# Performance work log

Measured on AMD Instinct MI355X. Metric: run time of the kernel, lower is better.

Reference implementation:

```python
import jax, jax.numpy as jnp
import numpy as np

N_NODES = 100000   # vertices
N_HEDGES = 20000   # hyperedges
NNZ = 1600000      # incidence entries (avg vertex degree 16)
IN_FT = 128
OUT_FT = 128


def setup_inputs() -> dict:
    key = jax.random.key(0)
    ks = jax.random.split(key, 8)
    stdv = 1.0 / np.sqrt(OUT_FT)
    x = jax.random.normal(ks[0], (N_NODES, IN_FT), dtype=jnp.float32)
    weight = jax.random.uniform(ks[1], (IN_FT, OUT_FT), dtype=jnp.float32, minval=-stdv, maxval=stdv)
    bias = jax.random.uniform(ks[2], (OUT_FT,), dtype=jnp.float32, minval=-stdv, maxval=stdv)
    node_idx = jax.random.randint(ks[3], (NNZ,), 0, N_NODES, dtype=jnp.int32)
    edge_idx = jax.random.randint(ks[4], (NNZ,), 0, N_HEDGES, dtype=jnp.int32)
    h_val = jnp.ones((NNZ,), dtype=jnp.float32)
    dv_inv = jax.random.uniform(ks[5], (N_NODES,), dtype=jnp.float32, minval=0.01, maxval=1.0)
    de_inv = jax.random.uniform(ks[6], (N_HEDGES,), dtype=jnp.float32, minval=0.01, maxval=1.0)
    return {"x": x, "weight": weight, "bias": bias, "node_idx": node_idx,
            "edge_idx": edge_idx, "h_val": h_val, "dv_inv": dv_inv, "de_inv": de_inv}


def reference(x, weight, bias, node_idx, edge_idx, h_val, dv_inv, de_inv):
    # dense map: X W + b
    x_mapped = jnp.matmul(x, weight) + bias                      # [N, F]
    # vertex-side degree scaling
    x_norm = x_mapped * dv_inv[:, None]                          # [N, F]
    # E = H^T x_norm : scatter vertex rows into hyperedges (spmm with COO H)
    msgs = x_norm[node_idx] * h_val[:, None]                     # [nnz, F]
    E = jax.ops.segment_sum(msgs, edge_idx, num_segments=N_HEDGES)  # [M, F]
    # hyperedge-side degree scaling
    E2 = E * de_inv[:, None]                                     # [M, F]
    # F_out = H E2 : scatter hyperedge rows back to vertices
    msgs2 = E2[edge_idx] * h_val[:, None]                        # [nnz, F]
    F_out = jax.ops.segment_sum(msgs2, node_idx, num_segments=N_NODES)  # [N, F]
    y = F_out * dv_inv[:, None]
    return y + x_mapped
```

## Files before the change

### kernel.cpp

```cpp
#include <hip/hip_runtime.h>


#define F 128
#define NBE 256
#define NBN 64
#define M_E 20000
#define RB_N 25000
#define R_N 4

__global__ __launch_bounds__(512) void kA_e(const int* __restrict__ ei,
                                            int* __restrict__ part2, int nnz) {
    __shared__ int sh[M_E];
    int b = blockIdx.x, t = threadIdx.x;
    for (int k = t; k < M_E; k += 512) sh[k] = 0;
    __syncthreads();
    int ch = (nnz + NBE - 1) / NBE;
    int i0 = b * ch, i1 = i0 + ch < nnz ? i0 + ch : nnz;
    for (int i = i0 + t; i < i1; i += 512) atomicAdd(&sh[ei[i]], 1);
    __syncthreads();
    for (int k = t; k < M_E; k += 512) part2[(size_t)b * M_E + k] = sh[k];
}

__global__ __launch_bounds__(512) void kA_n(const int* __restrict__ ni,
                                            int* __restrict__ partN2, int nnz) {
    __shared__ int sh[RB_N];
    int b = blockIdx.x >> 2, r = blockIdx.x & 3, t = threadIdx.x;
    for (int k = t; k < RB_N; k += 512) sh[k] = 0;
    __syncthreads();
    int ch = (nnz + NBN - 1) / NBN;
    int i0 = b * ch, i1 = i0 + ch < nnz ? i0 + ch : nnz;
    int lo = r * RB_N;
    for (int i = i0 + t; i < i1; i += 512) {
        int lb = ni[i] - lo;
        if ((unsigned)lb < (unsigned)RB_N) atomicAdd(&sh[lb], 1);
    }
    __syncthreads();
    for (int k = t; k < RB_N; k += 512)
        partN2[((size_t)(r * NBN + b)) * RB_N + k] = sh[k];
}

__global__ void kB(int* __restrict__ part2, int* __restrict__ cnt, int bins, int nb) {
    int bin = blockIdx.x * blockDim.x + threadIdx.x;
    if (bin >= bins) return;
    int run = 0;
#pragma unroll 8
    for (int b = 0; b < nb; ++b) {
        size_t idx = (size_t)b * bins + bin;
        int v = part2[idx];
        part2[idx] = run;
        run += v;
    }
    cnt[bin] = run;
}

__global__ void k_scan1(const int* __restrict__ cnt, int* __restrict__ excl,
                        int* __restrict__ part, int n) {
    __shared__ int s[256];
    int t = threadIdx.x;
    int base = blockIdx.x * 1024 + t * 4;
    int v0 = (base + 0 < n) ? cnt[base + 0] : 0;
    int v1 = (base + 1 < n) ? cnt[base + 1] : 0;
    int v2 = (base + 2 < n) ? cnt[base + 2] : 0;
    int v3 = (base + 3 < n) ? cnt[base + 3] : 0;
    s[t] = v0 + v1 + v2 + v3;
    __syncthreads();
    for (int off = 1; off < 256; off <<= 1) {
        int add = (t >= off) ? s[t - off] : 0;
        __syncthreads();
        s[t] += add;
        __syncthreads();
    }
    int r = (t > 0) ? s[t - 1] : 0;
    if (base + 0 < n) excl[base + 0] = r; r += v0;
    if (base + 1 < n) excl[base + 1] = r; r += v1;
    if (base + 2 < n) excl[base + 2] = r; r += v2;
    if (base + 3 < n) excl[base + 3] = r;
    if (t == 255) part[blockIdx.x] = s[255];
}

__global__ void k_scan2(int* __restrict__ part, int n) {
    __shared__ int s[256];
    int t = threadIdx.x;
    s[t] = (t < n) ? part[t] : 0;
    __syncthreads();
    for (int off = 1; off < 256; off <<= 1) {
        int add = (t >= off) ? s[t - off] : 0;
        __syncthreads();
        s[t] += add;
        __syncthreads();
    }
    if (t < n) part[t] = (t > 0) ? s[t - 1] : 0;
}

__global__ void k_scan3(int* __restrict__ start, const int* __restrict__ part, int n) {
    int i = blockIdx.x * blockDim.x + threadIdx.x;
    if (i < n) start[i] += part[i >> 10];
}

__global__ __launch_bounds__(512) void kC_e(const int* __restrict__ ei, const int* __restrict__ ni,
                                            const float* __restrict__ hv, const float* __restrict__ dv,
                                            const int* __restrict__ start, const int* __restrict__ part2,
                                            int2* __restrict__ eslot, int nnz) {
    __shared__ int sh[M_E];
    int b = blockIdx.x, t = threadIdx.x;
    for (int k = t; k < M_E; k += 512)
        sh[k] = start[k] + part2[(size_t)b * M_E + k];
    __syncthreads();
    int ch = (nnz + NBE - 1) / NBE;
    int i0 = b * ch, i1 = i0 + ch < nnz ? i0 + ch : nnz;
    for (int i = i0 + t; i < i1; i += 512) {
        int e = ei[i], nd = ni[i];
        float v = hv[i] * dv[nd];
        int p = atomicAdd(&sh[e], 1);
        eslot[p] = make_int2(nd, __float_as_int(v));
    }
}

__global__ __launch_bounds__(512) void kC_n(const int* __restrict__ ei, const int* __restrict__ ni,
                                            const float* __restrict__ hv,
                                            const int* __restrict__ start, const int* __restrict__ partN2,
                                            int2* __restrict__ nslot, int nnz) {
    __shared__ int sh[RB_N];
    int b = blockIdx.x >> 2, r = blockIdx.x & 3, t = threadIdx.x;
    int lo = r * RB_N;
    for (int k = t; k < RB_N; k += 512)
        sh[k] = start[lo + k] + partN2[((size_t)(r * NBN + b)) * RB_N + k];
    __syncthreads();
    int ch = (nnz + NBN - 1) / NBN;
    int i0 = b * ch, i1 = i0 + ch < nnz ? i0 + ch : nnz;
    for (int i = i0 + t; i < i1; i += 512) {
        int lb = ni[i] - lo;
        if ((unsigned)lb < (unsigned)RB_N) {
            int e = ei[i];
            float h = hv[i];
            int p = atomicAdd(&sh[lb], 1);
            nslot[p] = make_int2(e, __float_as_int(h));
        }
    }
}

__device__ __forceinline__ float f4_get(const float4& v, int k) {
    return k == 0 ? v.x : k == 1 ? v.y : k == 2 ? v.z : v.w;
}

__global__ __launch_bounds__(256) void k_gemm(const float* __restrict__ x,
                                              const float* __restrict__ w,
                                              const float* __restrict__ bias,
                                              float* __restrict__ y, int N) {
    __shared__ float sw[32 * 128];
    __shared__ float sx[128 * 36];
    int t = threadIdx.x;
    int row0 = blockIdx.x * 128;
    int cg = (t & 15) * 8;
    int rg = (t >> 4) * 8;
    float acc[8][8];
#pragma unroll
    for (int a = 0; a < 8; a++)
#pragma unroll
        for (int b = 0; b < 8; b++) acc[a][b] = 0.f;

    const float4* x4 = (const float4*)x;
    const float4* w4 = (const float4*)w;

    for (int kc = 0; kc < 4; ++kc) {
        __syncthreads();
        for (int i = t; i < 1024; i += 256) {
            int k = i >> 5, c4 = i & 31;
            ((float4*)sw)[i] = w4[(kc * 32 + k) * 32 + c4];
        }
        for (int i = t; i < 1024; i += 256) {
            int r = i >> 3, c4 = i & 7;
            float4 vv = make_float4(0.f, 0.f, 0.f, 0.f);
            if (row0 + r < N) vv = x4[(size_t)(row0 + r) * 32 + kc * 8 + c4];
            *(float4*)&sx[r * 36 + c4 * 4] = vv;
        }
        __syncthreads();
#pragma unroll
        for (int k4 = 0; k4 < 8; ++k4) {
            float4 xa[8];
#pragma unroll
            for (int rr = 0; rr < 8; rr++)
                xa[rr] = *(const float4*)&sx[(rg + rr) * 36 + k4 * 4];
#pragma unroll
            for (int kk = 0; kk < 4; kk++) {
                float4 wa0 = *(const float4*)&sw[(k4 * 4 + kk) * 128 + cg];
                float4 wa1 = *(const float4*)&sw[(k4 * 4 + kk) * 128 + cg + 4];
#pragma unroll
                for (int rr = 0; rr < 8; rr++) {
                    float xv = f4_get(xa[rr], kk);
                    acc[rr][0] += xv * wa0.x; acc[rr][1] += xv * wa0.y;
                    acc[rr][2] += xv * wa0.z; acc[rr][3] += xv * wa0.w;
                    acc[rr][4] += xv * wa1.x; acc[rr][5] += xv * wa1.y;
                    acc[rr][6] += xv * wa1.z; acc[rr][7] += xv * wa1.w;
                }
            }
        }
    }

    float4 b0 = *(const float4*)&bias[cg];
    float4 b1 = *(const float4*)&bias[cg + 4];
#pragma unroll
    for (int rr = 0; rr < 8; rr++) {
        int r = row0 + rg + rr;
        if (r < N) {
            float4 o0 = make_float4(acc[rr][0] + b0.x, acc[rr][1] + b0.y,
                                    acc[rr][2] + b0.z, acc[rr][3] + b0.w);
            float4 o1 = make_float4(acc[rr][4] + b1.x, acc[rr][5] + b1.y,
                                    acc[rr][6] + b1.z, acc[rr][7] + b1.w);
            *(float4*)&y[(size_t)r * F + cg]     = o0;
            *(float4*)&y[(size_t)r * F + cg + 4] = o1;
        }
    }
}

__global__ __launch_bounds__(256) void k_edge(const float* __restrict__ xm,
                                              const int2* __restrict__ slot,
                                              const float* __restrict__ de,
                                              const int* __restrict__ start,
                                              const int* __restrict__ cnt,
                                              float* __restrict__ E2, int M) {
    int wid = blockIdx.x * 4 + (threadIdx.x >> 6);
    if (wid >= M) return;
    int lane = threadIdx.x & 63;
    int hl = lane >> 5;
    int l  = lane & 31;
    int p = start[wid], c = cnt[wid];
    float a0 = 0.f, a1 = 0.f, a2 = 0.f, a3 = 0.f;
    int j = hl;
    for (; j + 2 < c; j += 4) {
        int2 s0 = slot[p + j];
        int2 s1 = slot[p + j + 2];
        float c0 = __int_as_float(s0.y), c1 = __int_as_float(s1.y);
        float4 v0 = *(const float4*)(xm + (size_t)s0.x * F + l * 4);
        float4 v1 = *(const float4*)(xm + (size_t)s1.x * F + l * 4);
        a0 += c0 * v0.x + c1 * v1.x;
        a1 += c0 * v0.y + c1 * v1.y;
        a2 += c0 * v0.z + c1 * v1.z;
        a3 += c0 * v0.w + c1 * v1.w;
    }
    if (j < c) {
        int2 s0 = slot[p + j];
        float c0 = __int_as_float(s0.y);
        float4 v0 = *(const float4*)(xm + (size_t)s0.x * F + l * 4);
        a0 += c0 * v0.x; a1 += c0 * v0.y; a2 += c0 * v0.z; a3 += c0 * v0.w;
    }
    a0 += __shfl_xor(a0, 32);
    a1 += __shfl_xor(a1, 32);
    a2 += __shfl_xor(a2, 32);
    a3 += __shfl_xor(a3, 32);
    if (hl == 0) {
        float s = de[wid];
        *(float4*)(E2 + (size_t)wid * F + l * 4) =
            make_float4(a0 * s, a1 * s, a2 * s, a3 * s);
    }
}

__global__ __launch_bounds__(256) void k_node(const float* xm,
                                              const int2* __restrict__ slot,
                                              const float* __restrict__ dv,
                                              const int* __restrict__ start,
                                              const int* __restrict__ cnt,
                                              const float* __restrict__ E2,
                                              float* out, int N) {
    int wid = blockIdx.x * 4 + (threadIdx.x >> 6);
    if (wid >= N) return;
    int lane = threadIdx.x & 63;
    int hl = lane >> 5;
    int l  = lane & 31;
    int p = start[wid], c = cnt[wid];
    float a0 = 0.f, a1 = 0.f, a2 = 0.f, a3 = 0.f;
    int j = hl;
    for (; j + 2 < c; j += 4) {
        int2 s0 = slot[p + j];
        int2 s1 = slot[p + j + 2];
        float c0 = __int_as_float(s0.y), c1 = __int_as_float(s1.y);
        float4 v0 = *(const float4*)(E2 + (size_t)s0.x * F + l * 4);
        float4 v1 = *(const float4*)(E2 + (size_t)s1.x * F + l * 4);
        a0 += c0 * v0.x + c1 * v1.x;
        a1 += c0 * v0.y + c1 * v1.y;
        a2 += c0 * v0.z + c1 * v1.z;
        a3 += c0 * v0.w + c1 * v1.w;
    }
    if (j < c) {
        int2 s0 = slot[p + j];
        float c0 = __int_as_float(s0.y);
        float4 v0 = *(const float4*)(E2 + (size_t)s0.x * F + l * 4);
        a0 += c0 * v0.x; a1 += c0 * v0.y; a2 += c0 * v0.z; a3 += c0 * v0.w;
    }
    a0 += __shfl_xor(a0, 32);
    a1 += __shfl_xor(a1, 32);
    a2 += __shfl_xor(a2, 32);
    a3 += __shfl_xor(a3, 32);
    if (hl == 0) {
        float dvn = dv[wid];
        float4 xv = *(const float4*)(xm + (size_t)wid * F + l * 4);
        *(float4*)(out + (size_t)wid * F + l * 4) =
            make_float4(a0 * dvn + xv.x, a1 * dvn + xv.y,
                        a2 * dvn + xv.z, a3 * dvn + xv.w);
    }
}

extern "C" void kernel_launch(void* const* d_in, const int* in_sizes, int n_in,
                              void* d_out, int out_size, void* d_ws, size_t ws_size,
                              hipStream_t stream) {
    const float* x      = (const float*)d_in[0];
    const float* w      = (const float*)d_in[1];
    const float* bias   = (const float*)d_in[2];
    const int*   ni     = (const int*)d_in[3];
    const int*   ei     = (const int*)d_in[4];
    const float* hv     = (const float*)d_in[5];
    const float* dv     = (const float*)d_in[6];
    const float* de     = (const float*)d_in[7];
    float* out = (float*)d_out;

    const int N   = in_sizes[0] / F;
    const int NNZ = in_sizes[3];
    const int M   = in_sizes[7];

    int* wsp        = (int*)d_ws;
    int* edge_cnt   = wsp;
    int* node_cnt   = edge_cnt + M;
    int* edge_start = node_cnt + N;
    int* node_start = edge_start + M;
    int* partE      = node_start + N;
    int* partN      = partE + 256;
    int* partE2     = partN + 256;
    int* partN2     = partE2 + (size_t)NBE * M_E;
    int2* eslot     = (int2*)(partN2 + (size_t)R_N * NBN * RB_N);
    int2* nslot     = eslot + NNZ;
    float* E2       = (float*)partN2;

    const int gScanE = (M + 1023) / 1024;
    const int gScanN = (N + 1023) / 1024;

    k_gemm<<<(N + 127) / 128, 256, 0, stream>>>(x, w, bias, out, N);

    kA_e<<<NBE, 512, 0, stream>>>(ei, partE2, NNZ);
    kA_n<<<NBN * R_N, 512, 0, stream>>>(ni, partN2, NNZ);

    kB<<<(M + 255) / 256, 256, 0, stream>>>(partE2, edge_cnt, M, NBE);
    for (int r = 0; r < R_N; ++r)
        kB<<<(RB_N + 255) / 256, 256, 0, stream>>>(partN2 + (size_t)r * NBN * RB_N,
                                                   node_cnt + (size_t)r * RB_N, RB_N, NBN);

    k_scan1<<<gScanE, 256, 0, stream>>>(edge_cnt, edge_start, partE, M);
    k_scan1<<<gScanN, 256, 0, stream>>>(node_cnt, node_start, partN, N);
    k_scan2<<<1, 256, 0, stream>>>(partE, gScanE);
    k_scan2<<<1, 256, 0, stream>>>(partN, gScanN);
    k_scan3<<<(M + 255) / 256, 256, 0, stream>>>(edge_start, partE, M);
    k_scan3<<<(N + 255) / 256, 256, 0, stream>>>(node_start, partN, N);

    kC_e<<<NBE, 512, 0, stream>>>(ei, ni, hv, dv, edge_start, partE2, eslot, NNZ);
    kC_n<<<NBN * R_N, 512, 0, stream>>>(ei, ni, hv, node_start, partN2, nslot, NNZ);

    k_edge<<<(M + 3) / 4, 256, 0, stream>>>(out, eslot, de, edge_start, edge_cnt, E2, M);
    k_node<<<(N + 3) / 4, 256, 0, stream>>>(out, nslot, dv, node_start, node_cnt, E2, out, N);
}
```

Measured before the change: 588.9 us.

## Gather bf16 copies of mapped features and edge sums in the SpMM passes

The GEMM now also writes a bf16 copy of X W + b, and the edge and node gather kernels read bf16 rows instead of fp32, which halves the bytes moved by the irregular gathers. The edge-pass output E2 is stored as bf16 too. To make room in the workspace, the GEMM launch moves after the CSR build and the edge histogram block count drops from 256 to 128. The risk is lost accuracy from bf16 rounding of the intermediates against the fp32 reference.

```diff
diff --git a/kernel.cpp b/kernel.cpp
--- a/kernel.cpp
+++ b/kernel.cpp
@@ -2,11 +2,20 @@
 
 
 #define F 128
-#define NBE 256
+#define NBE 128
 #define NBN 64
 #define M_E 20000
 #define RB_N 25000
 #define R_N 4
+
+__device__ __forceinline__ unsigned short f2bf(float f) {
+    unsigned u = __float_as_uint(f);
+    unsigned r = (u + 0x7FFF + ((u >> 16) & 1)) >> 16;
+    return (unsigned short)r;
+}
+__device__ __forceinline__ float bf2f(unsigned short h) {
+    return __uint_as_float((unsigned)h << 16);
+}
 
 __global__ __launch_bounds__(512) void kA_e(const int* __restrict__ ei,
                                             int* __restrict__ part2, int nnz) {
@@ -146,7 +155,8 @@
 __global__ __launch_bounds__(256) void k_gemm(const float* __restrict__ x,
                                               const float* __restrict__ w,
                                               const float* __restrict__ bias,
-                                              float* __restrict__ y, int N) {
+                                              float* __restrict__ y,
+                                              unsigned short* __restrict__ xmb, int N) {
     __shared__ float sw[32 * 128];
     __shared__ float sx[128 * 36];
     int t = threadIdx.x;
@@ -203,22 +213,26 @@
     for (int rr = 0; rr < 8; rr++) {
         int r = row0 + rg + rr;
         if (r < N) {
-            float4 o0 = make_float4(acc[rr][0] + b0.x, acc[rr][1] + b0.y,
-                                    acc[rr][2] + b0.z, acc[rr][3] + b0.w);
-            float4 o1 = make_float4(acc[rr][4] + b1.x, acc[rr][5] + b1.y,
-                                    acc[rr][6] + b1.z, acc[rr][7] + b1.w);
-            *(float4*)&y[(size_t)r * F + cg]     = o0;
-            *(float4*)&y[(size_t)r * F + cg + 4] = o1;
-        }
-    }
-}
-
-__global__ __launch_bounds__(256) void k_edge(const float* __restrict__ xm,
+            float o[8] = {acc[rr][0] + b0.x, acc[rr][1] + b0.y,
+                          acc[rr][2] + b0.z, acc[rr][3] + b0.w,
+                          acc[rr][4] + b1.x, acc[rr][5] + b1.y,
+                          acc[rr][6] + b1.z, acc[rr][7] + b1.w};
+            *(float4*)&y[(size_t)r * F + cg]     = make_float4(o[0], o[1], o[2], o[3]);
+            *(float4*)&y[(size_t)r * F + cg + 4] = make_float4(o[4], o[5], o[6], o[7]);
+            ushort4 h0 = {f2bf(o[0]), f2bf(o[1]), f2bf(o[2]), f2bf(o[3])};
+            ushort4 h1 = {f2bf(o[4]), f2bf(o[5]), f2bf(o[6]), f2bf(o[7])};
+            *(ushort4*)&xmb[(size_t)r * F + cg]     = h0;
+            *(ushort4*)&xmb[(size_t)r * F + cg + 4] = h1;
+        }
+    }
+}
+
+__global__ __launch_bounds__(256) void k_edge(const unsigned short* __restrict__ xmb,
                                               const int2* __restrict__ slot,
                                               const float* __restrict__ de,
                                               const int* __restrict__ start,
                                               const int* __restrict__ cnt,
-                                              float* __restrict__ E2, int M) {
+                                              unsigned short* __restrict__ E2b, int M) {
     int wid = blockIdx.x * 4 + (threadIdx.x >> 6);
     if (wid >= M) return;
     int lane = threadIdx.x & 63;
@@ -231,18 +245,19 @@
         int2 s0 = slot[p + j];
         int2 s1 = slot[p + j + 2];
         float c0 = __int_as_float(s0.y), c1 = __int_as_float(s1.y);
-        float4 v0 = *(const float4*)(xm + (size_t)s0.x * F + l * 4);
-        float4 v1 = *(const float4*)(xm + (size_t)s1.x * F + l * 4);
-        a0 += c0 * v0.x + c1 * v1.x;
-        a1 += c0 * v0.y + c1 * v1.y;
-        a2 += c0 * v0.z + c1 * v1.z;
-        a3 += c0 * v0.w + c1 * v1.w;
+        ushort4 v0 = *(const ushort4*)(xmb + (size_t)s0.x * F + l * 4);
+        ushort4 v1 = *(const ushort4*)(xmb + (size_t)s1.x * F + l * 4);
+        a0 += c0 * bf2f(v0.x) + c1 * bf2f(v1.x);
+        a1 += c0 * bf2f(v0.y) + c1 * bf2f(v1.y);
+        a2 += c0 * bf2f(v0.z) + c1 * bf2f(v1.z);
+        a3 += c0 * bf2f(v0.w) + c1 * bf2f(v1.w);
     }
     if (j < c) {
         int2 s0 = slot[p + j];
         float c0 = __int_as_float(s0.y);
-        float4 v0 = *(const float4*)(xm + (size_t)s0.x * F + l * 4);
-        a0 += c0 * v0.x; a1 += c0 * v0.y; a2 += c0 * v0.z; a3 += c0 * v0.w;
+        ushort4 v0 = *(const ushort4*)(xmb + (size_t)s0.x * F + l * 4);
+        a0 += c0 * bf2f(v0.x); a1 += c0 * bf2f(v0.y);
+        a2 += c0 * bf2f(v0.z); a3 += c0 * bf2f(v0.w);
     }
     a0 += __shfl_xor(a0, 32);
     a1 += __shfl_xor(a1, 32);
@@ -250,17 +265,16 @@
     a3 += __shfl_xor(a3, 32);
     if (hl == 0) {
         float s = de[wid];
-        *(float4*)(E2 + (size_t)wid * F + l * 4) =
-            make_float4(a0 * s, a1 * s, a2 * s, a3 * s);
-    }
-}
-
-__global__ __launch_bounds__(256) void k_node(const float* xm,
+        ushort4 o = {f2bf(a0 * s), f2bf(a1 * s), f2bf(a2 * s), f2bf(a3 * s)};
+        *(ushort4*)(E2b + (size_t)wid * F + l * 4) = o;
+    }
+}
+
+__global__ __launch_bounds__(256) void k_node(const unsigned short* __restrict__ E2b,
                                               const int2* __restrict__ slot,
                                               const float* __restrict__ dv,
                                               const int* __restrict__ start,
                                               const int* __restrict__ cnt,
-                                              const float* __restrict__ E2,
                                               float* out, int N) {
     int wid = blockIdx.x * 4 + (threadIdx.x >> 6);
     if (wid >= N) return;
@@ -274,18 +288,19 @@
         int2 s0 = slot[p + j];
         int2 s1 = slot[p + j + 2];
         float c0 = __int_as_float(s0.y), c1 = __int_as_float(s1.y);
-        float4 v0 = *(const float4*)(E2 + (size_t)s0.x * F + l * 4);
-        float4 v1 = *(const float4*)(E2 + (size_t)s1.x * F + l * 4);
-        a0 += c0 * v0.x + c1 * v1.x;
-        a1 += c0 * v0.y + c1 * v1.y;
-        a2 += c0 * v0.z + c1 * v1.z;
-        a3 += c0 * v0.w + c1 * v1.w;
+        ushort4 v0 = *(const ushort4*)(E2b + (size_t)s0.x * F + l * 4);
+        ushort4 v1 = *(const ushort4*)(E2b + (size_t)s1.x * F + l * 4);
+        a0 += c0 * bf2f(v0.x) + c1 * bf2f(v1.x);
+        a1 += c0 * bf2f(v0.y) + c1 * bf2f(v1.y);
+        a2 += c0 * bf2f(v0.z) + c1 * bf2f(v1.z);
+        a3 += c0 * bf2f(v0.w) + c1 * bf2f(v1.w);
     }
     if (j < c) {
         int2 s0 = slot[p + j];
         float c0 = __int_as_float(s0.y);
-        float4 v0 = *(const float4*)(E2 + (size_t)s0.x * F + l * 4);
-        a0 += c0 * v0.x; a1 += c0 * v0.y; a2 += c0 * v0.z; a3 += c0 * v0.w;
+        ushort4 v0 = *(const ushort4*)(E2b + (size_t)s0.x * F + l * 4);
+        a0 += c0 * bf2f(v0.x); a1 += c0 * bf2f(v0.y);
+        a2 += c0 * bf2f(v0.z); a3 += c0 * bf2f(v0.w);
     }
     a0 += __shfl_xor(a0, 32);
     a1 += __shfl_xor(a1, 32);
@@ -293,7 +308,7 @@
     a3 += __shfl_xor(a3, 32);
     if (hl == 0) {
         float dvn = dv[wid];
-        float4 xv = *(const float4*)(xm + (size_t)wid * F + l * 4);
+        float4 xv = *(const float4*)(out + (size_t)wid * F + l * 4);
         *(float4*)(out + (size_t)wid * F + l * 4) =
             make_float4(a0 * dvn + xv.x, a1 * dvn + xv.y,
                         a2 * dvn + xv.z, a3 * dvn + xv.w);
@@ -328,12 +343,11 @@
     int* partN2     = partE2 + (size_t)NBE * M_E;
     int2* eslot     = (int2*)(partN2 + (size_t)R_N * NBN * RB_N);
     int2* nslot     = eslot + NNZ;
-    float* E2       = (float*)partN2;
+    unsigned short* xmb = (unsigned short*)partN2;
+    unsigned short* E2b = (unsigned short*)partE2;
 
     const int gScanE = (M + 1023) / 1024;
     const int gScanN = (N + 1023) / 1024;
-
-    k_gemm<<<(N + 127) / 128, 256, 0, stream>>>(x, w, bias, out, N);
 
     kA_e<<<NBE, 512, 0, stream>>>(ei, partE2, NNZ);
     kA_n<<<NBN * R_N, 512, 0, stream>>>(ni, partN2, NNZ);
@@ -353,6 +367,8 @@
     kC_e<<<NBE, 512, 0, stream>>>(ei, ni, hv, dv, edge_start, partE2, eslot, NNZ);
     kC_n<<<NBN * R_N, 512, 0, stream>>>(ei, ni, hv, node_start, partN2, nslot, NNZ);
 
-    k_edge<<<(M + 3) / 4, 256, 0, stream>>>(out, eslot, de, edge_start, edge_cnt, E2, M);
-    k_node<<<(N + 3) / 4, 256, 0, stream>>>(out, nslot, dv, node_start, node_cnt, E2, out, N);
-}
+    k_gemm<<<(N + 127) / 128, 256, 0, stream>>>(x, w, bias, out, xmb, N);
+
+    k_edge<<<(M + 3) / 4, 256, 0, stream>>>(xmb, eslot, de, edge_start, edge_cnt, E2b, M);
+    k_node<<<(N + 3) / 4, 256, 0, stream>>>(E2b, nslot, dv, node_start, node_cnt, out, N);
+}
```

Measured after the change: 523.8 us. 11.0% less time.
